# Performance work log

Hardware: AMD Instinct MI355X
Metric: run time of the kernel (lower is better)

The kernel has to match this reference:

```python
import jax, jax.numpy as jnp
import numpy as np

N_VARS = 32
D_MODEL = 256
D_MECH = 128
D_NOISE = D_MODEL // 4
N_LAYERS = 3
TEMP = 0.5
BATCH = 512


def gelu(x):
    return jax.nn.gelu(x, approximate=False)  # torch nn.GELU default is exact erf


def setup_inputs() -> dict:
    key = jax.random.key(0)
    ks = jax.random.split(key, 12)
    n, d, m, dn = N_VARS, D_MODEL, D_MECH, D_NOISE
    return {
        "exogenous_noise": jax.random.normal(ks[0], (BATCH, n, dn), dtype=jnp.float32),
        # learned params (edge_logits init randn*0.5 for a nontrivial adjacency)
        "edge_logits": jax.random.normal(ks[1], (n, n), dtype=jnp.float32) * 0.5,
        "var_emb": jax.random.normal(ks[2], (n, d), dtype=jnp.float32) * 0.02,
        # shared parent_aggregate Linear(d, d); weights stored [in, out]
        "pa_W": jax.random.normal(ks[3], (d, d), dtype=jnp.float32) / np.sqrt(d).astype(np.float32),
        "pa_b": jnp.zeros((d,), dtype=jnp.float32),
        # per-variable mechanism MLP weights, stacked on variable axis
        "m_W1": jax.random.normal(ks[4], (n, d, m), dtype=jnp.float32) / np.sqrt(d).astype(np.float32),
        "m_b1": jnp.zeros((n, m), dtype=jnp.float32),
        "m_W2": jax.random.normal(ks[5], (n, m, m), dtype=jnp.float32) / np.sqrt(m).astype(np.float32),
        "m_b2": jnp.zeros((n, m), dtype=jnp.float32),
        "m_W3": jax.random.normal(ks[6], (n, m, d), dtype=jnp.float32) / np.sqrt(m).astype(np.float32),
        "m_b3": jnp.zeros((n, d), dtype=jnp.float32),
        # per-variable noise encoder Linear(dn, d)
        "ne_W": jax.random.normal(ks[7], (n, dn, d), dtype=jnp.float32) / np.sqrt(dn).astype(np.float32),
        "ne_b": jnp.zeros((n, d), dtype=jnp.float32),
    }


def _forward(exogenous_noise, edge_logits, var_emb, pa_W, pa_b,
             m_W1, m_b1, m_W2, m_b2, m_W3, m_b3, ne_W, ne_b):
    n, d = N_VARS, D_MODEL
    batch = exogenous_noise.shape[0]
    # eval-mode adjacency: sigmoid(masked_logits / temp); diagonal masked out
    diag_mask = 1.0 - jnp.eye(n, dtype=edge_logits.dtype)
    adj = jax.nn.sigmoid((edge_logits * diag_mask) / jnp.asarray(TEMP, edge_logits.dtype))
    adj_cols = adj.T                                  # row i = adj[:, i], parents of var i
    noise_t = jnp.transpose(exogenous_noise, (1, 0, 2))  # (n, batch, dn)

    values0 = jnp.zeros((batch, n, d), dtype=exogenous_noise.dtype)
    idx = jnp.arange(n)
    xs = (idx, adj_cols, var_emb, noise_t, m_W1, m_b1, m_W2, m_b2, m_W3, m_b3, ne_W, ne_b)

    def var_step(values, x):
        i, a_col, emb_i, nz, w1, b1, w2, b2, w3, b3, nw, nb = x
        # adjacency-weighted aggregation over ALL current values (sequentially updated)
        pc = jnp.einsum('v,bvd->bd', a_col, values)
        parent_input = gelu((pc + emb_i) @ pa_W + pa_b)
        h = gelu(parent_input @ w1 + b1)
        h = gelu(h @ w2 + b2)
        out = h @ w3 + b3
        out = out + gelu(nz @ nw + nb)               # noise encoder contribution
        values = values.at[:, i].set(out)
        return values, None

    values = values0
    for _ in range(N_LAYERS):
        values, _ = jax.lax.scan(var_step, values, xs)
    return values


def reference(exogenous_noise, edge_logits, var_emb, pa_W, pa_b,
              m_W1, m_b1, m_W2, m_b2, m_W3, m_b3, ne_W, ne_b):
    return _forward(exogenous_noise, edge_logits, var_emb, pa_W, pa_b,
                    m_W1, m_b1, m_W2, m_b2, m_W3, m_b3, ne_W, ne_b)
```

## Files before the change

### kernel.cpp

```cpp
#include <hip/hip_runtime.h>


typedef __bf16 bf16x8 __attribute__((ext_vector_type(8)));
typedef float  f32x4  __attribute__((ext_vector_type(4)));

#define N_VARS 32
#define BTILE 4
#define NBLK 128

#define ELOFF_PA 0
#define ELOFF_W1 65536
#define ELOFF_W2 1114112
#define ELOFF_W3 1638400

#define XSTR 272
#define HSTR 144

__device__ __forceinline__ unsigned short f2b(float f) {
    unsigned u = __float_as_uint(f);
    u += 0x7FFFu + ((u >> 16) & 1u);
    return (unsigned short)(u >> 16);
}

__device__ __forceinline__ void bar_lds() {
    asm volatile("s_waitcnt lgkmcnt(0)\n\ts_barrier" ::: "memory");
}

__device__ __forceinline__ float gelu_e(float x) {
    float z  = x * 0.7071067811865476f;
    float az = fabsf(z);
    float t  = __builtin_amdgcn_rcpf(1.0f + 0.47047f * az);
    float p  = t * (0.3480242f + t * (-0.0958798f + t * 0.7478556f));
    float e  = 1.0f - p * __expf(-z * z);
    float er = (z < 0.0f) ? -e : e;
    return 0.5f * x * (1.0f + er);
}

__device__ __forceinline__ float pickq(f32x4 v, int q) {
    float lo = (q & 1) ? v[1] : v[0];
    float hi = (q & 1) ? v[3] : v[2];
    return (q & 2) ? hi : lo;
}

__global__ void prep_all(const float* __restrict__ paW, const float* __restrict__ mW1,
                         const float* __restrict__ mW2, const float* __restrict__ mW3,
                         const float* __restrict__ edge, unsigned short* __restrict__ wsb,
                         float* __restrict__ adjT,
                         const float* __restrict__ noise, const float* __restrict__ neW,
                         const float* __restrict__ neb, float* __restrict__ outp) {
    __shared__ unsigned short tile[32 * 256];
    const int c = blockIdx.x, tid = threadIdx.x;
    if (c < 520) {
        const float* src; unsigned short* dst; int N, KS, ks;
        if (c < 8)        { src = paW;                     dst = wsb + ELOFF_PA;             N = 256; KS = 8; ks = c; }
        else if (c < 264) { int v = (c - 8) >> 3;   ks = (c - 8) & 7;
                            src = mW1 + v * 32768;         dst = wsb + ELOFF_W1 + v * 32768; N = 128; KS = 8; }
        else if (c < 392) { int v = (c - 264) >> 2; ks = (c - 264) & 3;
                            src = mW2 + v * 16384;         dst = wsb + ELOFF_W2 + v * 16384; N = 128; KS = 4; }
        else              { int v = (c - 392) >> 2; ks = (c - 392) & 3;
                            src = mW3 + v * 32768;         dst = wsb + ELOFF_W3 + v * 32768; N = 256; KS = 4; }
        const int kb = ks * 32, nsh = (N == 256) ? 8 : 7;
        for (int t = tid; t < 32 * N; t += 256) {
            int r = t >> nsh, col = t & (N - 1);
            tile[r * N + col] = f2b(src[(kb + r) * N + col]);
        }
        __syncthreads();
        const int nout = (N >> 4) * 64;
        for (int o = tid; o < nout; o += 256) {
            int nt = o >> 6, lane = o & 63;
            int n = nt * 16 + (lane & 15), k0 = (lane >> 4) << 3;
            unsigned e[8];
            #pragma unroll
            for (int j = 0; j < 8; j++) e[j] = tile[(k0 + j) * N + n];
            uint4 pk;
            pk.x = e[0] | (e[1] << 16); pk.y = e[2] | (e[3] << 16);
            pk.z = e[4] | (e[5] << 16); pk.w = e[6] | (e[7] << 16);
            *(uint4*)(dst + ((nt * KS + ks) * 64 + lane) * 8) = pk;
        }
    } else if (c == 520) {
        for (int t = tid; t < 1024; t += 256) {
            int v = t >> 5, ci = t & 31;
            float x = edge[t];
            float m = (v == ci) ? 0.0f : x;
            adjT[ci * 32 + v] = __builtin_amdgcn_rcpf(1.0f + __expf(-2.0f * m));
        }
    } else {
        int sb = c - 521;
        int i = sb >> 5, g = sb & 31, d = tid;
        float w[64];
        #pragma unroll
        for (int k = 0; k < 64; k++) w[k] = neW[(i * 64 + k) * 256 + d];
        float bias = neb[i * 256 + d];
        for (int bb = 0; bb < 16; bb++) {
            int b = g * 16 + bb;
            const float* nr = noise + (b * 32 + i) * 64;
            float a0 = bias, a1 = 0.f, a2 = 0.f, a3 = 0.f;
            #pragma unroll
            for (int k = 0; k < 16; k++) {
                a0 += nr[4 * k + 0] * w[4 * k + 0];
                a1 += nr[4 * k + 1] * w[4 * k + 1];
                a2 += nr[4 * k + 2] * w[4 * k + 2];
                a3 += nr[4 * k + 3] * w[4 * k + 3];
            }
            outp[(b * 32 + i) * 256 + d] = gelu_e((a0 + a1) + (a2 + a3));
        }
    }
}

#define MFMA16(a, b, c) __builtin_amdgcn_mfma_f32_16x16x32_bf16(a, b, c, 0, 0, 0)

__global__ __launch_bounds__(512) void
scm_main(const float* __restrict__ emb, const float* __restrict__ pab,
         const float* __restrict__ mb1, const float* __restrict__ mb2,
         const float* __restrict__ mb3, const float* __restrict__ adjT,
         const __bf16* __restrict__ wsbf, float* __restrict__ outp) {
    __shared__ unsigned short valsS[32 * 1024];
    __shared__ unsigned short Xs[4 * XSTR];
    __shared__ unsigned short X2[4 * XSTR];
    __shared__ unsigned short Hs1[4 * HSTR];
    __shared__ unsigned short Hs2[4 * HSTR];

    const int tid = threadIdx.x, blk = blockIdx.x;

    {
        uint4 z; z.x = z.y = z.z = z.w = 0;
        for (int k = tid; k < 4096; k += 512) ((uint4*)valsS)[k] = z;
    }

    const int wid = tid >> 6, lane = tid & 63, l15 = lane & 15, q = lane >> 4;
    const int l3 = l15 & 3;
    const int nW = wid * 16 + l15;
    const int n0 = nW, n1 = nW + 128;
    const int rE = tid >> 7, cE = tid & 127;

    const float pb0 = pab[n0], pb1 = pab[n1];

    bf16x8 paf0[8], paf1[8];
    #pragma unroll
    for (int ks = 0; ks < 8; ks++) {
        paf0[ks] = *(const bf16x8*)(wsbf + ELOFF_PA + ((wid * 8 + ks) * 64 + lane) * 8);
        paf1[ks] = *(const bf16x8*)(wsbf + ELOFF_PA + (((wid + 8) * 8 + ks) * 64 + lane) * 8);
    }

    {
        float2 e0 = *(const float2*)(emb + cE * 2);
        *(unsigned*)(Xs + rE * XSTR + cE * 2) =
            (unsigned)f2b(e0.x) | ((unsigned)f2b(e0.y) << 16);
    }
    bar_lds();

    for (int s = 0; s < 3 * N_VARS; s++) {
        const int i = s & 31, ni = (s + 1) & 31;
        const bool last = s >= 64;
        const float* __restrict__ an = adjT + ni * 32;

        float bi1 = mb1[i * 128 + nW];
        float bi2 = mb2[i * 128 + nW];
        float b3a = mb3[i * 256 + n0];
        float b3b = mb3[i * 256 + n1];
        bf16x8 w1f[8];
        #pragma unroll
        for (int ks = 0; ks < 8; ks++)
            w1f[ks] = *(const bf16x8*)(wsbf + ELOFF_W1 + (size_t)i * 32768 +
                                       ((wid * 8 + ks) * 64 + lane) * 8);
        bf16x8 w2f[4], w3f0[4], w3f1[4];
        #pragma unroll
        for (int ks = 0; ks < 4; ks++) {
            w2f[ks]  = *(const bf16x8*)(wsbf + ELOFF_W2 + (size_t)i * 16384 +
                                        ((wid * 4 + ks) * 64 + lane) * 8);
            w3f0[ks] = *(const bf16x8*)(wsbf + ELOFF_W3 + (size_t)i * 32768 +
                                        ((wid * 4 + ks) * 64 + lane) * 8);
            w3f1[ks] = *(const bf16x8*)(wsbf + ELOFF_W3 + (size_t)i * 32768 +
                                        (((wid + 8) * 4 + ks) * 64 + lane) * 8);
        }
        const size_t obq = ((size_t)(blk * BTILE + q) * 32 + i) * 256;
        const float neq0 = outp[obq + n0];
        const float neq1 = outp[obq + n1];

        {
            f32x4 a0e = {0, 0, 0, 0}, a0o = {0, 0, 0, 0};
            f32x4 a1e = {0, 0, 0, 0}, a1o = {0, 0, 0, 0};
            #pragma unroll
            for (int ks = 0; ks < 8; ks += 2) {
                bf16x8 af0 = *(const bf16x8*)(Xs + l3 * XSTR + ks * 32 + q * 8);
                bf16x8 af1 = *(const bf16x8*)(Xs + l3 * XSTR + (ks + 1) * 32 + q * 8);
                a0e = MFMA16(af0, paf0[ks], a0e);
                a1e = MFMA16(af0, paf1[ks], a1e);
                a0o = MFMA16(af1, paf0[ks + 1], a0o);
                a1o = MFMA16(af1, paf1[ks + 1], a1o);
            }
            float s0 = pickq(a0e, q) + pickq(a0o, q) + pb0;
            float s1 = pickq(a1e, q) + pickq(a1o, q) + pb1;
            X2[q * XSTR + n0] = f2b(gelu_e(s0));
            X2[q * XSTR + n1] = f2b(gelu_e(s1));
        }
        bar_lds();

        float p0 = 0.f, p1 = 0.f, of0, of1;
        {
            f32x4 aa = {0, 0, 0, 0}, ab = {0, 0, 0, 0};
            f32x4 ac = {0, 0, 0, 0}, ad = {0, 0, 0, 0};
            #pragma unroll
            for (int ks = 0; ks < 8; ks += 4) {
                bf16x8 af0 = *(const bf16x8*)(X2 + l3 * XSTR + ks * 32 + q * 8);
                bf16x8 af1 = *(const bf16x8*)(X2 + l3 * XSTR + (ks + 1) * 32 + q * 8);
                bf16x8 af2 = *(const bf16x8*)(X2 + l3 * XSTR + (ks + 2) * 32 + q * 8);
                bf16x8 af3 = *(const bf16x8*)(X2 + l3 * XSTR + (ks + 3) * 32 + q * 8);
                aa = MFMA16(af0, w1f[ks], aa);
                ab = MFMA16(af1, w1f[ks + 1], ab);
                ac = MFMA16(af2, w1f[ks + 2], ac);
                ad = MFMA16(af3, w1f[ks + 3], ad);
            }
            const unsigned short* vp = valsS + rE * 256 + cE * 2;
            #pragma unroll
            for (int v = 0; v < 16; v++) {
                unsigned u = *(const unsigned*)(vp + v * 1024);
                float sc = an[v];
                p0 += sc * __uint_as_float(u << 16);
                p1 += sc * __uint_as_float(u & 0xFFFF0000u);
            }
            {
                unsigned uo = *(const unsigned*)(valsS + i * 1024 + rE * 256 + cE * 2);
                of0 = __uint_as_float(uo << 16);
                of1 = __uint_as_float(uo & 0xFFFF0000u);
            }
            float sb = (pickq(aa, q) + pickq(ab, q)) +
                       (pickq(ac, q) + pickq(ad, q)) + bi1;
            Hs1[q * HSTR + nW] = f2b(gelu_e(sb));
        }
        bar_lds();

        float2 e2n = *(const float2*)(emb + ni * 256 + cE * 2);
        {
            f32x4 ca = {0, 0, 0, 0}, cb = {0, 0, 0, 0};
            #pragma unroll
            for (int ks = 0; ks < 4; ks += 2) {
                bf16x8 af0 = *(const bf16x8*)(Hs1 + l3 * HSTR + ks * 32 + q * 8);
                bf16x8 af1 = *(const bf16x8*)(Hs1 + l3 * HSTR + (ks + 1) * 32 + q * 8);
                ca = MFMA16(af0, w2f[ks], ca);
                cb = MFMA16(af1, w2f[ks + 1], cb);
            }
            const unsigned short* vp = valsS + rE * 256 + cE * 2;
            #pragma unroll
            for (int v = 16; v < 32; v++) {
                unsigned u = *(const unsigned*)(vp + v * 1024);
                float sc = an[v];
                p0 += sc * __uint_as_float(u << 16);
                p1 += sc * __uint_as_float(u & 0xFFFF0000u);
            }
            float scv = pickq(ca, q) + pickq(cb, q) + bi2;
            Hs2[q * HSTR + nW] = f2b(gelu_e(scv));
        }
        bar_lds();

        {
            f32x4 c0a = {0, 0, 0, 0}, c0b = {0, 0, 0, 0};
            f32x4 c1a = {0, 0, 0, 0}, c1b = {0, 0, 0, 0};
            #pragma unroll
            for (int ks = 0; ks < 4; ks += 2) {
                bf16x8 af0 = *(const bf16x8*)(Hs2 + l3 * HSTR + ks * 32 + q * 8);
                bf16x8 af1 = *(const bf16x8*)(Hs2 + l3 * HSTR + (ks + 1) * 32 + q * 8);
                c0a = MFMA16(af0, w3f0[ks], c0a);
                c1a = MFMA16(af0, w3f1[ks], c1a);
                c0b = MFMA16(af1, w3f0[ks + 1], c0b);
                c1b = MFMA16(af1, w3f1[ks + 1], c1b);
            }
            float v0 = pickq(c0a, q) + pickq(c0b, q) + b3a + neq0;
            float v1 = pickq(c1a, q) + pickq(c1b, q) + b3b + neq1;
            valsS[i * 1024 + q * 256 + n0] = f2b(v0);
            valsS[i * 1024 + q * 256 + n1] = f2b(v1);
            if (last) {
                outp[obq + n0] = v0;
                outp[obq + n1] = v1;
            }
        }
        bar_lds();

        {
            unsigned un = *(const unsigned*)(valsS + i * 1024 + rE * 256 + cE * 2);
            float av = an[i];
            float x0 = p0 + av * (__uint_as_float(un << 16)          - of0) + e2n.x;
            float x1 = p1 + av * (__uint_as_float(un & 0xFFFF0000u)  - of1) + e2n.y;
            *(unsigned*)(Xs + rE * XSTR + cE * 2) =
                (unsigned)f2b(x0) | ((unsigned)f2b(x1) << 16);
        }
        bar_lds();
    }
}

extern "C" void kernel_launch(void* const* d_in, const int* in_sizes, int n_in,
                              void* d_out, int out_size, void* d_ws, size_t ws_size,
                              hipStream_t stream) {
    (void)in_sizes; (void)n_in; (void)out_size; (void)ws_size;
    const float* noise = (const float*)d_in[0];
    const float* edge  = (const float*)d_in[1];
    const float* emb   = (const float*)d_in[2];
    const float* paW   = (const float*)d_in[3];
    const float* pab   = (const float*)d_in[4];
    const float* mW1   = (const float*)d_in[5];
    const float* mb1   = (const float*)d_in[6];
    const float* mW2   = (const float*)d_in[7];
    const float* mb2   = (const float*)d_in[8];
    const float* mW3   = (const float*)d_in[9];
    const float* mb3   = (const float*)d_in[10];
    const float* neW   = (const float*)d_in[11];
    const float* neb   = (const float*)d_in[12];
    float* outp = (float*)d_out;

    float* adjT = (float*)d_ws;
    unsigned short* wsb = (unsigned short*)((char*)d_ws + 4096);

    prep_all<<<1545, 256, 0, stream>>>(paW, mW1, mW2, mW3, edge, wsb, adjT,
                                       noise, neW, neb, outp);
    scm_main<<<NBLK, 512, 0, stream>>>(emb, pab, mb1, mb2, mb3, adjT,
                                       (const __bf16*)wsb, outp);
}
```

Measured before the change: 387.7 us.

## Compute adjacency aggregation with MFMA on transposed value layout, drop a barrier

The parent aggregation over all 32 variable values used to be a scalar FMA loop reading per-variable rows of shared memory. It is now done with bf16 MFMAs against a transposed, padded values layout. The adjacency is split into hi and lo bf16 parts to keep precision close to fp32. The next-step X build now runs in the same phase as the value store, removing one barrier per step, but it needs two MFMAs per tile and scalar scattered LDS writes into the transposed layout.

```diff
diff --git a/kernel.cpp b/kernel.cpp
--- a/kernel.cpp
+++ b/kernel.cpp
@@ -15,11 +15,16 @@
 
 #define XSTR 272
 #define HSTR 144
+#define VSTR 40
 
 __device__ __forceinline__ unsigned short f2b(float f) {
     unsigned u = __float_as_uint(f);
     u += 0x7FFFu + ((u >> 16) & 1u);
     return (unsigned short)(u >> 16);
+}
+
+__device__ __forceinline__ float b2f(unsigned short u) {
+    return __uint_as_float(((unsigned)u) << 16);
 }
 
 __device__ __forceinline__ void bar_lds() {
@@ -41,11 +46,16 @@
     float hi = (q & 1) ? v[3] : v[2];
     return (q & 2) ? hi : lo;
 }
+__device__ __forceinline__ float pick4(float x0, float x1, float x2, float x3, int q) {
+    float lo = (q & 1) ? x1 : x0;
+    float hi = (q & 1) ? x3 : x2;
+    return (q & 2) ? hi : lo;
+}
 
 __global__ void prep_all(const float* __restrict__ paW, const float* __restrict__ mW1,
                          const float* __restrict__ mW2, const float* __restrict__ mW3,
                          const float* __restrict__ edge, unsigned short* __restrict__ wsb,
-                         float* __restrict__ adjT,
+                         unsigned short* __restrict__ adjb,
                          const float* __restrict__ noise, const float* __restrict__ neW,
                          const float* __restrict__ neb, float* __restrict__ outp) {
     __shared__ unsigned short tile[32 * 256];
@@ -82,7 +92,11 @@
             int v = t >> 5, ci = t & 31;
             float x = edge[t];
             float m = (v == ci) ? 0.0f : x;
-            adjT[ci * 32 + v] = __builtin_amdgcn_rcpf(1.0f + __expf(-2.0f * m));
+            float a = __builtin_amdgcn_rcpf(1.0f + __expf(-2.0f * m));
+            unsigned short hi = f2b(a);
+            float rem = a - b2f(hi);
+            adjb[ci * 64 + v]      = hi;
+            adjb[ci * 64 + 32 + v] = f2b(rem);
         }
     } else {
         int sb = c - 521;
@@ -112,9 +126,9 @@
 __global__ __launch_bounds__(512) void
 scm_main(const float* __restrict__ emb, const float* __restrict__ pab,
          const float* __restrict__ mb1, const float* __restrict__ mb2,
-         const float* __restrict__ mb3, const float* __restrict__ adjT,
+         const float* __restrict__ mb3, const unsigned short* __restrict__ adjb,
          const __bf16* __restrict__ wsbf, float* __restrict__ outp) {
-    __shared__ unsigned short valsS[32 * 1024];
+    __shared__ unsigned short valsT[1024 * VSTR];
     __shared__ unsigned short Xs[4 * XSTR];
     __shared__ unsigned short X2[4 * XSTR];
     __shared__ unsigned short Hs1[4 * HSTR];
@@ -124,14 +138,13 @@
 
     {
         uint4 z; z.x = z.y = z.z = z.w = 0;
-        for (int k = tid; k < 4096; k += 512) ((uint4*)valsS)[k] = z;
+        for (int k = tid; k < 5120; k += 512) ((uint4*)valsT)[k] = z;
     }
 
     const int wid = tid >> 6, lane = tid & 63, l15 = lane & 15, q = lane >> 4;
     const int l3 = l15 & 3;
     const int nW = wid * 16 + l15;
     const int n0 = nW, n1 = nW + 128;
-    const int rE = tid >> 7, cE = tid & 127;
 
     const float pb0 = pab[n0], pb1 = pab[n1];
 
@@ -142,17 +155,13 @@
         paf1[ks] = *(const bf16x8*)(wsbf + ELOFF_PA + (((wid + 8) * 8 + ks) * 64 + lane) * 8);
     }
 
-    {
-        float2 e0 = *(const float2*)(emb + cE * 2);
-        *(unsigned*)(Xs + rE * XSTR + cE * 2) =
-            (unsigned)f2b(e0.x) | ((unsigned)f2b(e0.y) << 16);
-    }
+    Xs[q * XSTR + n0] = f2b(emb[n0]);
+    Xs[q * XSTR + n1] = f2b(emb[n1]);
     bar_lds();
 
     for (int s = 0; s < 3 * N_VARS; s++) {
         const int i = s & 31, ni = (s + 1) & 31;
         const bool last = s >= 64;
-        const float* __restrict__ an = adjT + ni * 32;
 
         float bi1 = mb1[i * 128 + nW];
         float bi2 = mb2[i * 128 + nW];
@@ -176,6 +185,11 @@
         const size_t obq = ((size_t)(blk * BTILE + q) * 32 + i) * 256;
         const float neq0 = outp[obq + n0];
         const float neq1 = outp[obq + n1];
+        bf16x8 anh = *(const bf16x8*)(adjb + ni * 64 + q * 8);
+        bf16x8 anl = *(const bf16x8*)(adjb + ni * 64 + 32 + q * 8);
+        const float ani = b2f(adjb[ni * 64 + i]) + b2f(adjb[ni * 64 + 32 + i]);
+        const float e0 = emb[ni * 256 + n0];
+        const float e1 = emb[ni * 256 + n1];
 
         {
             f32x4 a0e = {0, 0, 0, 0}, a0o = {0, 0, 0, 0};
@@ -196,7 +210,6 @@
         }
         bar_lds();
 
-        float p0 = 0.f, p1 = 0.f, of0, of1;
         {
             f32x4 aa = {0, 0, 0, 0}, ab = {0, 0, 0, 0};
             f32x4 ac = {0, 0, 0, 0}, ad = {0, 0, 0, 0};
@@ -211,26 +224,14 @@
                 ac = MFMA16(af2, w1f[ks + 2], ac);
                 ad = MFMA16(af3, w1f[ks + 3], ad);
             }
-            const unsigned short* vp = valsS + rE * 256 + cE * 2;
-            #pragma unroll
-            for (int v = 0; v < 16; v++) {
-                unsigned u = *(const unsigned*)(vp + v * 1024);
-                float sc = an[v];
-                p0 += sc * __uint_as_float(u << 16);
-                p1 += sc * __uint_as_float(u & 0xFFFF0000u);
-            }
-            {
-                unsigned uo = *(const unsigned*)(valsS + i * 1024 + rE * 256 + cE * 2);
-                of0 = __uint_as_float(uo << 16);
-                of1 = __uint_as_float(uo & 0xFFFF0000u);
-            }
             float sb = (pickq(aa, q) + pickq(ab, q)) +
                        (pickq(ac, q) + pickq(ad, q)) + bi1;
             Hs1[q * HSTR + nW] = f2b(gelu_e(sb));
         }
         bar_lds();
 
-        float2 e2n = *(const float2*)(emb + ni * 256 + cE * 2);
+        f32x4 P0[4], P1[4];
+        float o0, o1;
         {
             f32x4 ca = {0, 0, 0, 0}, cb = {0, 0, 0, 0};
             #pragma unroll
@@ -240,14 +241,16 @@
                 ca = MFMA16(af0, w2f[ks], ca);
                 cb = MFMA16(af1, w2f[ks + 1], cb);
             }
-            const unsigned short* vp = valsS + rE * 256 + cE * 2;
-            #pragma unroll
-            for (int v = 16; v < 32; v++) {
-                unsigned u = *(const unsigned*)(vp + v * 1024);
-                float sc = an[v];
-                p0 += sc * __uint_as_float(u << 16);
-                p1 += sc * __uint_as_float(u & 0xFFFF0000u);
-            }
+            #pragma unroll
+            for (int t = 0; t < 4; t++) {
+                bf16x8 vf0 = *(const bf16x8*)(valsT + (t * 256 + n0) * VSTR + q * 8);
+                bf16x8 vf1 = *(const bf16x8*)(valsT + (t * 256 + n1) * VSTR + q * 8);
+                f32x4 z = {0, 0, 0, 0};
+                P0[t] = MFMA16(anl, vf0, MFMA16(anh, vf0, z));
+                P1[t] = MFMA16(anl, vf1, MFMA16(anh, vf1, z));
+            }
+            o0 = b2f(valsT[(q * 256 + n0) * VSTR + i]);
+            o1 = b2f(valsT[(q * 256 + n1) * VSTR + i]);
             float scv = pickq(ca, q) + pickq(cb, q) + bi2;
             Hs2[q * HSTR + nW] = f2b(gelu_e(scv));
         }
@@ -267,22 +270,19 @@
             }
             float v0 = pickq(c0a, q) + pickq(c0b, q) + b3a + neq0;
             float v1 = pickq(c1a, q) + pickq(c1b, q) + b3b + neq1;
-            valsS[i * 1024 + q * 256 + n0] = f2b(v0);
-            valsS[i * 1024 + q * 256 + n1] = f2b(v1);
+            unsigned short ur0 = f2b(v0), ur1 = f2b(v1);
+            valsT[(q * 256 + n0) * VSTR + i] = ur0;
+            valsT[(q * 256 + n1) * VSTR + i] = ur1;
             if (last) {
                 outp[obq + n0] = v0;
                 outp[obq + n1] = v1;
             }
-        }
-        bar_lds();
-
-        {
-            unsigned un = *(const unsigned*)(valsS + i * 1024 + rE * 256 + cE * 2);
-            float av = an[i];
-            float x0 = p0 + av * (__uint_as_float(un << 16)          - of0) + e2n.x;
-            float x1 = p1 + av * (__uint_as_float(un & 0xFFFF0000u)  - of1) + e2n.y;
-            *(unsigned*)(Xs + rE * XSTR + cE * 2) =
-                (unsigned)f2b(x0) | ((unsigned)f2b(x1) << 16);
+            float pc0 = pick4(P0[0][0], P0[1][0], P0[2][0], P0[3][0], q);
+            float pc1 = pick4(P1[0][0], P1[1][0], P1[2][0], P1[3][0], q);
+            float x0 = pc0 + ani * (b2f(ur0) - o0) + e0;
+            float x1 = pc1 + ani * (b2f(ur1) - o1) + e1;
+            Xs[q * XSTR + n0] = f2b(x0);
+            Xs[q * XSTR + n1] = f2b(x1);
         }
         bar_lds();
     }
@@ -307,11 +307,11 @@
     const float* neb   = (const float*)d_in[12];
     float* outp = (float*)d_out;
 
-    float* adjT = (float*)d_ws;
-    unsigned short* wsb = (unsigned short*)((char*)d_ws + 4096);
-
-    prep_all<<<1545, 256, 0, stream>>>(paW, mW1, mW2, mW3, edge, wsb, adjT,
+    unsigned short* adjb = (unsigned short*)d_ws;
+    unsigned short* wsb  = (unsigned short*)((char*)d_ws + 4096);
+
+    prep_all<<<1545, 256, 0, stream>>>(paW, mW1, mW2, mW3, edge, wsb, adjb,
                                        noise, neW, neb, outp);
-    scm_main<<<NBLK, 512, 0, stream>>>(emb, pab, mb1, mb2, mb3, adjT,
+    scm_main<<<NBLK, 512, 0, stream>>>(emb, pab, mb1, mb2, mb3, adjb,
                                        (const __bf16*)wsb, outp);
 }
```

Result: faster. 373.5 us (-3.7%).
